# Kernel optimization log

Hardware: AMD Instinct MI355X
Metric: run time of the kernel (lower is better)

## Reference

```python
import jax, jax.numpy as jnp
import numpy as np

EPS_BN = 1e-5
NEG_SLOPE = 0.2
N_GRAPHS = 64


def _gat_layer(x, src, dst, W, att_s, att_d, b, concat):
    # x: [N, Fin]; W: [Fin, H*C]; att_s/att_d: [H, C]; PyG GATConv semantics
    N = x.shape[0]
    H, C = att_s.shape
    h = (x @ W).reshape(N, H, C)                      # [N,H,C]
    a_s = jnp.einsum('nhc,hc->nh', h, att_s)          # per-node src score
    a_d = jnp.einsum('nhc,hc->nh', h, att_d)          # per-node dst score
    e = jax.nn.leaky_relu(a_s[src] + a_d[dst], NEG_SLOPE)  # [E,H]
    m = jax.ops.segment_max(e, dst, num_segments=N)   # segment softmax over incoming edges
    ex = jnp.exp(e - m[dst])
    den = jax.ops.segment_sum(ex, dst, num_segments=N)
    alpha = ex / (den[dst] + 1e-16)                   # [E,H]
    msg = h[src] * alpha[:, :, None]                  # [E,H,C]
    out = jax.ops.segment_sum(msg, dst, num_segments=N)
    out = out.reshape(N, H * C) if concat else out.mean(axis=1)
    return out + b


def _bn(x, g, bt):
    mu = x.mean(axis=0)
    var = x.var(axis=0)
    return (x - mu) * jax.lax.rsqrt(var + EPS_BN) * g + bt


def setup_inputs() -> dict:
    key = jax.random.key(0)
    ks = jax.random.split(key, 32)
    N, E, F = 50000, 800000, 128
    d = {}
    d['x'] = jax.random.normal(ks[0], (N, F), dtype=jnp.float32)
    d['edge_index'] = jax.random.randint(ks[1], (2, E), 0, N, dtype=jnp.int32)
    d['batch'] = jnp.sort(jax.random.randint(ks[2], (N,), 0, N_GRAPHS, dtype=jnp.int32))
    def p(k, shape, fan):
        return jax.random.normal(k, shape, dtype=jnp.float32) * (1.0 / np.sqrt(fan))
    d['W1'] = p(ks[3], (128, 256), 128); d['as1'] = p(ks[4], (4, 64), 64)
    d['ad1'] = p(ks[5], (4, 64), 64); d['b1'] = jnp.zeros((256,), jnp.float32)
    d['W2'] = p(ks[6], (256, 128), 256); d['as2'] = p(ks[7], (4, 32), 32)
    d['ad2'] = p(ks[8], (4, 32), 32); d['b2'] = jnp.zeros((128,), jnp.float32)
    # gat3: 128 -> 64, 1 head, mean
    d['W3'] = p(ks[9], (128, 64), 128); d['as3'] = p(ks[10], (1, 64), 64)
    d['ad3'] = p(ks[11], (1, 64), 64); d['b3'] = jnp.zeros((64,), jnp.float32)
    # batch norms
    d['g1'] = jnp.ones((256,), jnp.float32); d['bt1'] = jnp.zeros((256,), jnp.float32)
    d['g2'] = jnp.ones((128,), jnp.float32); d['bt2'] = jnp.zeros((128,), jnp.float32)
    d['g3'] = jnp.ones((64,), jnp.float32); d['bt3'] = jnp.zeros((64,), jnp.float32)
    # fcn: 64 -> 128 -> 32 -> 2
    d['fw1'] = p(ks[12], (64, 128), 64); d['fb1'] = jnp.zeros((128,), jnp.float32)
    d['fw2'] = p(ks[13], (128, 32), 128); d['fb2'] = jnp.zeros((32,), jnp.float32)
    d['fw3'] = p(ks[14], (32, 2), 32); d['fb3'] = jnp.zeros((2,), jnp.float32)
    return d


def reference(x, edge_index, batch, W1, as1, ad1, b1, W2, as2, ad2, b2,
              W3, as3, ad3, b3, g1, bt1, g2, bt2, g3, bt3,
              fw1, fb1, fw2, fb2, fw3, fb3):
    N = x.shape[0]
    # add self loops (PyG GATConv default)
    loops = jnp.arange(N, dtype=edge_index.dtype)
    src = jnp.concatenate([edge_index[0], loops])
    dst = jnp.concatenate([edge_index[1], loops])
    h = _gat_layer(x, src, dst, W1, as1, ad1, b1, concat=True)
    h = jax.nn.elu(_bn(h, g1, bt1))
    h = _gat_layer(h, src, dst, W2, as2, ad2, b2, concat=True)
    h = jax.nn.elu(_bn(h, g2, bt2))
    h = _gat_layer(h, src, dst, W3, as3, ad3, b3, concat=False)
    h = jax.nn.elu(_bn(h, g3, bt3))
    # global mean pool per graph
    s = jax.ops.segment_sum(h, batch, num_segments=N_GRAPHS)
    cnt = jax.ops.segment_sum(jnp.ones((N,), h.dtype), batch, num_segments=N_GRAPHS)
    pooled = s / jnp.maximum(cnt, 1.0)[:, None]       # [64, 64]
    z = jax.nn.leaky_relu(pooled @ fw1 + fb1, NEG_SLOPE)
    z = jax.nn.leaky_relu(z @ fw2 + fb2, NEG_SLOPE)
    return z @ fw3 + fb3                              # [64, 2]
```

## Files before the change

### kernel.cpp

```cpp
#include <hip/hip_runtime.h>
#include <hip/hip_fp16.h>
#include <math.h>

#define NEG_SLOPE 0.2f
#define BN_NB 128
#define BK_SHIFT 6
#define BK_CAP 2048
#define SC_CHUNK 4096

typedef _Float16 f16x8 __attribute__((ext_vector_type(8)));
typedef float    f32x4 __attribute__((ext_vector_type(4)));


__device__ inline void scan1024_incl(int* tmp) {
    int t = threadIdx.x;
    for (int off = 1; off < 1024; off <<= 1) {
        int vals[4];
#pragma unroll
        for (int k = 0; k < 4; k++) {
            int idx = t + k * 256;
            vals[k] = (idx >= off) ? tmp[idx - off] : 0;
        }
        __syncthreads();
#pragma unroll
        for (int k = 0; k < 4; k++) tmp[t + k * 256] += vals[k];
        __syncthreads();
    }
}

__global__ __launch_bounds__(256) void histA_kernel(const int* __restrict__ dst,
                                                    int* __restrict__ bcnt, int E, int nb) {
    __shared__ int h[1024];
    int t = threadIdx.x;
    for (int i = t; i < 1024; i += 256) h[i] = 0;
    __syncthreads();
    int base = blockIdx.x * SC_CHUNK;
#pragma unroll 4
    for (int k = 0; k < SC_CHUNK / 256; k++) {
        int i = base + t + k * 256;
        if (i < E) atomicAdd(&h[dst[i] >> BK_SHIFT], 1);
    }
    __syncthreads();
    for (int i = t; i < nb; i += 256) if (h[i]) atomicAdd(&bcnt[i], h[i]);
}

__global__ __launch_bounds__(256) void scanAB_kernel(const int* __restrict__ bcnt,
                                                     int* __restrict__ boffs,
                                                     int* __restrict__ gcurs, int nb) {
    __shared__ int tmp[1024];
    int t = threadIdx.x;
    for (int i = t; i < 1024; i += 256) tmp[i] = (i < nb) ? bcnt[i] : 0;
    __syncthreads();
    scan1024_incl(tmp);
    for (int i = t; i < nb; i += 256) {
        int excl = (i == 0) ? 0 : tmp[i - 1];
        boffs[i] = excl;
        gcurs[i] = excl;
    }
    if (t == 0) boffs[nb] = tmp[nb - 1];
}

__global__ __launch_bounds__(256) void scatterB_kernel(const int* __restrict__ src,
                                                       const int* __restrict__ dst,
                                                       int* __restrict__ gcurs,
                                                       unsigned* __restrict__ ebuf,
                                                       int E, int nb) {
    __shared__ int hcnt[1024];
    __shared__ int hcur[1024];
    __shared__ int gbase[1024];
    __shared__ unsigned stage[SC_CHUNK];
    __shared__ unsigned short sbk[SC_CHUNK];
    int t = threadIdx.x;
    int base = blockIdx.x * SC_CHUNK;
    for (int i = t; i < 1024; i += 256) hcnt[i] = 0;
    __syncthreads();
    unsigned pk[SC_CHUNK / 256];
    int bk[SC_CHUNK / 256];
#pragma unroll
    for (int k = 0; k < SC_CHUNK / 256; k++) {
        int i = base + t + k * 256;
        if (i < E) {
            int d = dst[i];
            int s = src[i];
            bk[k] = d >> BK_SHIFT;
            pk[k] = (unsigned)s | ((unsigned)(d & 63) << 16);
            atomicAdd(&hcnt[bk[k]], 1);
        } else bk[k] = -1;
    }
    __syncthreads();
    for (int i = t; i < 1024; i += 256) hcur[i] = hcnt[i];
    __syncthreads();
    scan1024_incl(hcur);
    for (int i = t; i < 1024; i += 256) hcur[i] -= hcnt[i];
    __syncthreads();
#pragma unroll
    for (int k = 0; k < SC_CHUNK / 256; k++) {
        if (bk[k] >= 0) {
            int p = atomicAdd(&hcur[bk[k]], 1);
            stage[p] = pk[k];
            sbk[p] = (unsigned short)bk[k];
        }
    }
    __syncthreads();
    for (int i = t; i < nb; i += 256) {
        int c = hcnt[i];
        gbase[i] = c ? atomicAdd(&gcurs[i], c) : 0;
    }
    __syncthreads();
    int total = E - base; if (total > SC_CHUNK) total = SC_CHUNK;
    for (int i = t; i < total; i += 256) {
        int b = sbk[i];
        int local = i - (hcur[b] - hcnt[b]);
        ebuf[gbase[b] + local] = stage[i];
    }
}

__global__ __launch_bounds__(256) void buildC_kernel(const unsigned* __restrict__ ebuf,
                                                     const int* __restrict__ boffs,
                                                     int* __restrict__ offs,
                                                     int* __restrict__ csrc, int N) {
    __shared__ int ncnt[64], ncur[64];
    __shared__ int npre[65];
    __shared__ unsigned lv[BK_CAP];
    __shared__ int lout[BK_CAP];
    int b = blockIdx.x, t = threadIdx.x;
    int e0 = boffs[b], e1 = boffs[b + 1];
    int cnt = e1 - e0; if (cnt > BK_CAP) cnt = BK_CAP;
    int n0 = b << BK_SHIFT;
    if (t < 64) ncnt[t] = 0;
    __syncthreads();
    for (int i = t; i < cnt; i += 256) {
        unsigned v = ebuf[e0 + i];
        lv[i] = v;
        atomicAdd(&ncnt[v >> 16], 1);
    }
    __syncthreads();
    if (t == 0) {
        int run = 0;
#pragma unroll
        for (int i = 0; i < 64; i++) { npre[i] = run; run += ncnt[i]; }
        npre[64] = run;
    }
    __syncthreads();
    int nEnd = N - n0; if (nEnd > 64) nEnd = 64;
    if (t < nEnd) offs[n0 + t + 1] = e0 + npre[t + 1];
    if (b == 0 && t == 0) offs[0] = 0;
    if (t < 64) ncur[t] = npre[t];
    __syncthreads();
    for (int i = t; i < cnt; i += 256) {
        unsigned v = lv[i];
        int p = atomicAdd(&ncur[v >> 16], 1);
        lout[p] = (int)(v & 0xFFFFu);
    }
    __syncthreads();
    for (int i = t; i < cnt; i += 256) csrc[e0 + i] = lout[i];
}


__device__ inline void swz1(const float* __restrict__ W, __half* __restrict__ Wsw,
                            int Nout, int i) {
    int k = i / Nout, n = i % Nout;
    Wsw[((size_t)(k >> 3) * Nout + n) * 8 + (k & 7)] = __float2half(W[i]);
}

__global__ void prep_kernel(const float* __restrict__ W1, const float* __restrict__ W2,
                            const float* __restrict__ W3,
                            const float* __restrict__ as1, const float* __restrict__ ad1,
                            __half* __restrict__ W1sw, __half* __restrict__ W2sw,
                            __half* __restrict__ W3sw, float* __restrict__ wsd,
                            const float* __restrict__ x, __half* __restrict__ Xh,
                            int castN4) {
    int i = blockIdx.x * 256 + threadIdx.x;
    const int R0 = 128 * 256, R1 = R0 + 256 * 128, R2 = R1 + 128 * 64, R3 = R2 + 1024;
    if (i < R0) { swz1(W1, W1sw, 256, i); }
    else if (i < R1) { swz1(W2, W2sw, 128, i - R0); }
    else if (i < R2) { swz1(W3, W3sw, 64, i - R1); }
    else if (i < R3) {
        int j = (i - R2) >> 7, k = (i - R2) & 127;
        int hh = j & 3;
        const float* att = (j < 4) ? as1 : ad1;
        float s = 0.f;
        for (int c = 0; c < 64; c++) s += W1[k * 256 + hh * 64 + c] * att[hh * 64 + c];
        wsd[i - R2] = s;
    } else {
        int j = i - R3;
        if (j < castN4) {
            float4 v = *(const float4*)(x + (size_t)j * 4);
            __half2 pk[2];
            pk[0] = __floats2half2_rn(v.x, v.y);
            pk[1] = __floats2half2_rn(v.z, v.w);
            *(uint2*)(Xh + (size_t)j * 4) = *(uint2*)pk;
        }
    }
}


__global__ __launch_bounds__(256) void scores1_kernel(const __half* __restrict__ Xh,
                                                      const float* __restrict__ wsd,
                                                      float* __restrict__ a_s,
                                                      float* __restrict__ a_d, int N) {
    int gid = blockIdx.x * 256 + threadIdx.x;
    if (gid >= N * 8) return;
    int n = gid >> 3, j = gid & 7;
    const __half* xp = Xh + (size_t)n * 128;
    const float* wp = wsd + j * 128;
    float s = 0.f;
    for (int k = 0; k < 128; k += 8) {
        uint4 raw = *(const uint4*)(xp + k);
        __half2* hp = (__half2*)&raw;
#pragma unroll
        for (int q = 0; q < 4; q++) {
            float2 f = __half22float2(hp[q]);
            s += f.x * wp[k + 2 * q] + f.y * wp[k + 2 * q + 1];
        }
    }
    if (j < 4) a_s[n * 4 + j] = s; else a_d[n * 4 + (j - 4)] = s;
}


__global__ __launch_bounds__(256) void aggx_kernel(const __half* __restrict__ Xh,
                                                   const float* __restrict__ a_s,
                                                   const float* __restrict__ a_d,
                                                   const int* __restrict__ offs,
                                                   const int* __restrict__ csrc,
                                                   __half* __restrict__ aggx, int N) {
    __shared__ float wbuf[16][16 * 4];
    __shared__ int   sbuf[16][16];
    int tid = threadIdx.x;
    int l16 = tid & 15, grp = tid >> 4;
    int node = blockIdx.x * 16 + grp;
    if (node >= N) return;
    int off = offs[node];
    int deg = offs[node + 1] - off;
    float4 ad4 = *(const float4*)(a_d + (size_t)node * 4);
    float adl[4] = {ad4.x, ad4.y, ad4.z, ad4.w};
    float4 as4 = *(const float4*)(a_s + (size_t)node * 4);
    float asl[4] = {as4.x, as4.y, as4.z, as4.w};
    float wself[4];
#pragma unroll
    for (int h = 0; h < 4; h++) {
        float sc = asl[h] + adl[h];
        sc = sc > 0.f ? sc : NEG_SLOPE * sc;
        wself[h] = __expf(sc);
    }
    float acc[4][8];
    {
        uint4 raw = *(const uint4*)(Xh + (size_t)node * 128 + l16 * 8);
        __half2* p = (__half2*)&raw;
#pragma unroll
        for (int q = 0; q < 4; q++) {
            float2 f = __half22float2(p[q]);
#pragma unroll
            for (int h = 0; h < 4; h++) {
                acc[h][2 * q] = wself[h] * f.x;
                acc[h][2 * q + 1] = wself[h] * f.y;
            }
        }
    }
    float denp[4] = {0.f, 0.f, 0.f, 0.f};
    for (int base = 0; base < deg; base += 16) {
        int i = base + l16;
        if (i < deg) {
            int s = csrc[off + i];
            sbuf[grp][l16] = s;
            float4 t4 = *(const float4*)(a_s + (size_t)s * 4);
            float asv[4] = {t4.x, t4.y, t4.z, t4.w};
#pragma unroll
            for (int h = 0; h < 4; h++) {
                float sc = asv[h] + adl[h];
                sc = sc > 0.f ? sc : NEG_SLOPE * sc;
                float w = __expf(sc);
                wbuf[grp][l16 * 4 + h] = w;
                denp[h] += w;
            }
        }
        asm volatile("s_waitcnt lgkmcnt(0)" ::: "memory");
        int cl = deg - base; if (cl > 16) cl = 16;
#pragma unroll 4
        for (int e = 0; e < cl; e++) {
            int s = sbuf[grp][e];
            float4 wv = *(float4*)&wbuf[grp][e * 4];
            float wa[4] = {wv.x, wv.y, wv.z, wv.w};
            uint4 raw = *(const uint4*)(Xh + (size_t)s * 128 + l16 * 8);
            __half2* p = (__half2*)&raw;
#pragma unroll
            for (int q = 0; q < 4; q++) {
                float2 f = __half22float2(p[q]);
#pragma unroll
                for (int h = 0; h < 4; h++) {
                    acc[h][2 * q] += wa[h] * f.x;
                    acc[h][2 * q + 1] += wa[h] * f.y;
                }
            }
        }
    }
#pragma unroll
    for (int d = 1; d <= 8; d <<= 1)
#pragma unroll
        for (int h = 0; h < 4; h++) denp[h] += __shfl_xor(denp[h], d, 64);
#pragma unroll
    for (int h = 0; h < 4; h++) {
        float inv = 1.0f / (denp[h] + wself[h] + 1e-16f);
        uint4 pk; __half2* q = (__half2*)&pk;
#pragma unroll
        for (int j = 0; j < 4; j++)
            q[j] = __floats2half2_rn(acc[h][2 * j] * inv, acc[h][2 * j + 1] * inv);
        *(uint4*)(aggx + (size_t)node * 512 + h * 128 + l16 * 8) = pk;
    }
}


template <int CH, bool BN, bool SCORES, bool BIAS>
__global__ __launch_bounds__(256) void gemm_mfma(const __half* __restrict__ X,
                                                 const __half* __restrict__ Wsw,
                                                 __half* __restrict__ Yh,
                                                 const float* __restrict__ att_s,
                                                 const float* __restrict__ att_d,
                                                 float* __restrict__ a_s,
                                                 float* __restrict__ a_d,
                                                 const float* __restrict__ partials,
                                                 const float* __restrict__ gbn,
                                                 const float* __restrict__ btbn,
                                                 const float* __restrict__ bias,
                                                 float invN, int aStride, int aOffPerBn,
                                                 int M, int K, int Nout) {
    extern __shared__ char smem_raw[];
    __half* Bs = (__half*)smem_raw;
    float* ssc = (float*)(smem_raw + (size_t)K * 64 * 2);
    float* ssb = ssc + K;
    int tid = threadIdx.x;
    int wave = tid >> 6, lane = tid & 63;
    int bm = blockIdx.x * 128;
    int bn = blockIdx.y * 64;

    if (BN && tid < K) {
        float ssum = 0.f, qsum = 0.f;
        for (int b = 0; b < BN_NB; b++) {
            ssum += partials[(size_t)b * 2 * K + tid];
            qsum += partials[(size_t)b * 2 * K + K + tid];
        }
        float mu = ssum * invN;
        float var = qsum * invN - mu * mu;
        float sc = gbn[tid] * rsqrtf(var + 1e-5f);
        ssc[tid] = sc;
        ssb[tid] = btbn[tid] - mu * sc;
    }

    int ktCount = K >> 3;
    int totalVec = ktCount * 64;
    for (int i = tid; i < totalVec; i += 256) {
        int kt = i >> 6, off = i & 63;
        ((uint4*)Bs)[i] = *(const uint4*)(Wsw + ((size_t)kt * Nout + bn + off) * 8);
    }
    __syncthreads();

    int quad = lane >> 4, l15 = lane & 15;
    int row0 = bm + wave * 32 + l15;
    bool r0ok = (row0 < M), r1ok = (row0 + 16 < M);
    int aOff = blockIdx.y * aOffPerBn;
    const __half* a0p = X + (size_t)row0 * aStride + aOff + quad * 8;
    const __half* a1p = a0p + (size_t)16 * aStride;

    f32x4 acc[2][4] = {};
    for (int kstep = 0; kstep < K; kstep += 32) {
        f16x8 a0 = {}, a1 = {};
        if (r0ok) a0 = *(const f16x8*)(a0p + kstep);
        if (r1ok) a1 = *(const f16x8*)(a1p + kstep);
        if (BN) {
            int c0 = kstep + quad * 8;
#pragma unroll
            for (int j = 0; j < 8; j++) {
                float sc = ssc[c0 + j], sb = ssb[c0 + j];
                float v0 = (float)a0[j] * sc + sb;
                v0 = v0 > 0.f ? v0 : (__expf(v0) - 1.0f);
                a0[j] = (_Float16)v0;
                float v1 = (float)a1[j] * sc + sb;
                v1 = v1 > 0.f ? v1 : (__expf(v1) - 1.0f);
                a1[j] = (_Float16)v1;
            }
        }
        int ktbase = (kstep >> 3) + quad;
#pragma unroll
        for (int nt = 0; nt < 4; nt++) {
            f16x8 b = *(const f16x8*)(Bs + ((size_t)ktbase * 64 + nt * 16 + l15) * 8);
            acc[0][nt] = __builtin_amdgcn_mfma_f32_16x16x32_f16(a0, b, acc[0][nt], 0, 0, 0);
            acc[1][nt] = __builtin_amdgcn_mfma_f32_16x16x32_f16(a1, b, acc[1][nt], 0, 0, 0);
        }
    }

    float bv[4];
    if (BIAS) {
#pragma unroll
        for (int nt = 0; nt < 4; nt++) bv[nt] = bias[bn + nt * 16 + l15];
    }

#pragma unroll
    for (int mt = 0; mt < 2; mt++) {
#pragma unroll
        for (int r = 0; r < 4; r++) {
            int row = bm + wave * 32 + mt * 16 + quad * 4 + r;
            if (row < M) {
#pragma unroll
                for (int nt = 0; nt < 4; nt++) {
                    float v = acc[mt][nt][r];
                    if (BIAS) v += bv[nt];
                    Yh[(size_t)row * Nout + bn + nt * 16 + l15] = __float2half(v);
                }
            }
        }
    }

    if (SCORES) {
        constexpr int LH = 64 / CH;
        const int H = Nout / CH;
        float as_l[4], ad_l[4];
#pragma unroll
        for (int nt = 0; nt < 4; nt++) {
            int gcol = bn + nt * 16 + l15;
            as_l[nt] = att_s[gcol];
            ad_l[nt] = att_d[gcol];
        }
        float ps[2][4][LH], pd[2][4][LH];
#pragma unroll
        for (int mt = 0; mt < 2; mt++)
#pragma unroll
            for (int r = 0; r < 4; r++)
#pragma unroll
                for (int lh = 0; lh < LH; lh++) { ps[mt][r][lh] = 0.f; pd[mt][r][lh] = 0.f; }
#pragma unroll
        for (int mt = 0; mt < 2; mt++)
#pragma unroll
            for (int nt = 0; nt < 4; nt++) {
                int lh = (nt * 16) / CH;
#pragma unroll
                for (int r = 0; r < 4; r++) {
                    ps[mt][r][lh] += acc[mt][nt][r] * as_l[nt];
                    pd[mt][r][lh] += acc[mt][nt][r] * ad_l[nt];
                }
            }
#pragma unroll
        for (int d = 1; d <= 8; d <<= 1) {
#pragma unroll
            for (int mt = 0; mt < 2; mt++)
#pragma unroll
                for (int r = 0; r < 4; r++)
#pragma unroll
                    for (int lh = 0; lh < LH; lh++) {
                        ps[mt][r][lh] += __shfl_xor(ps[mt][r][lh], d, 64);
                        pd[mt][r][lh] += __shfl_xor(pd[mt][r][lh], d, 64);
                    }
        }
        if (l15 == 0) {
#pragma unroll
            for (int mt = 0; mt < 2; mt++)
#pragma unroll
                for (int r = 0; r < 4; r++) {
                    int row = bm + wave * 32 + mt * 16 + quad * 4 + r;
                    if (row < M) {
#pragma unroll
                        for (int lh = 0; lh < LH; lh++) {
                            int ghead = bn / CH + lh;
                            a_s[(size_t)row * H + ghead] = ps[mt][r][lh];
                            a_d[(size_t)row * H + ghead] = pd[mt][r][lh];
                        }
                    }
                }
        }
    }
}


template <int H, int C>
__global__ __launch_bounds__(256) void agg_kernel(const __half* __restrict__ h,
                                                  const float* __restrict__ a_s,
                                                  const float* __restrict__ a_d,
                                                  const int* __restrict__ offs,
                                                  const int* __restrict__ csrc,
                                                  const float* __restrict__ bias,
                                                  __half* __restrict__ out, int N) {
    const int HC = H * C;
    const int CPL = HC / 16;
    __shared__ float wbuf[16][16 * H];
    __shared__ int   sbuf[16][16];
    int tid = threadIdx.x;
    int l16 = tid & 15;
    int grp = tid >> 4;
    int node = blockIdx.x * 16 + grp;
    if (node >= N) return;
    int off = offs[node];
    int deg = offs[node + 1] - off;
    int mych = l16 * CPL;
    int mh   = mych / C;

    float adl[H];
#pragma unroll
    for (int hh = 0; hh < H; hh++) adl[hh] = a_d[node * H + hh];

    float acc[CPL];
    float sc_self = a_s[node * H + mh] + adl[mh];
    sc_self = sc_self > 0.f ? sc_self : NEG_SLOPE * sc_self;
    float w_self = __expf(sc_self);
    {
        const __half* hp = h + (size_t)node * HC + mych;
        if (CPL == 8) {
            uint4 r0 = *(const uint4*)hp;
            __half2* p0 = (__half2*)&r0;
#pragma unroll
            for (int j = 0; j < 4; j++) {
                float2 f = __half22float2(p0[j]);
                acc[2 * j] = w_self * f.x; acc[2 * j + 1] = w_self * f.y;
            }
        } else {
            uint2 r0 = *(const uint2*)hp;
            __half2* p0 = (__half2*)&r0;
#pragma unroll
            for (int j = 0; j < 2; j++) {
                float2 f = __half22float2(p0[j]);
                acc[2 * j] = w_self * f.x; acc[2 * j + 1] = w_self * f.y;
            }
        }
    }

    float denp[H];
#pragma unroll
    for (int hh = 0; hh < H; hh++) denp[hh] = 0.f;

    for (int base = 0; base < deg; base += 16) {
        int i = base + l16;
        if (i < deg) {
            int s = csrc[off + i];
            sbuf[grp][l16] = s;
            float asv[H];
            if (H == 4) {
                float4 t4 = *(const float4*)(a_s + (size_t)s * 4);
                asv[0] = t4.x; asv[1] = t4.y; asv[2] = t4.z; asv[3] = t4.w;
            } else {
                asv[0] = a_s[s];
            }
#pragma unroll
            for (int hh = 0; hh < H; hh++) {
                float sc = asv[hh] + adl[hh];
                sc = sc > 0.f ? sc : NEG_SLOPE * sc;
                float w = __expf(sc);
                wbuf[grp][l16 * H + hh] = w;
                denp[hh] += w;
            }
        }
        asm volatile("s_waitcnt lgkmcnt(0)" ::: "memory");
        int cl = deg - base; if (cl > 16) cl = 16;
#pragma unroll 4
        for (int e = 0; e < cl; e++) {
            int s = sbuf[grp][e];
            float w = wbuf[grp][e * H + mh];
            const __half* hp = h + (size_t)s * HC + mych;
            if (CPL == 8) {
                uint4 r0 = *(const uint4*)hp;
                __half2* p0 = (__half2*)&r0;
#pragma unroll
                for (int j = 0; j < 4; j++) {
                    float2 f = __half22float2(p0[j]);
                    acc[2 * j] += w * f.x; acc[2 * j + 1] += w * f.y;
                }
            } else {
                uint2 r0 = *(const uint2*)hp;
                __half2* p0 = (__half2*)&r0;
#pragma unroll
                for (int j = 0; j < 2; j++) {
                    float2 f = __half22float2(p0[j]);
                    acc[2 * j] += w * f.x; acc[2 * j + 1] += w * f.y;
                }
            }
        }
    }
#pragma unroll
    for (int d = 1; d <= 8; d <<= 1) {
#pragma unroll
        for (int hh = 0; hh < H; hh++)
            denp[hh] += __shfl_xor(denp[hh], d, 64);
    }
    float inv = 1.0f / (denp[mh] + w_self + 1e-16f);
    {
        __half* op = out + (size_t)node * HC + mych;
        if (CPL == 8) {
            uint4 pk;
            __half2* q = (__half2*)&pk;
#pragma unroll
            for (int j = 0; j < 4; j++)
                q[j] = __floats2half2_rn(acc[2 * j] * inv + bias[mych + 2 * j],
                                         acc[2 * j + 1] * inv + bias[mych + 2 * j + 1]);
            *(uint4*)op = pk;
        } else {
            uint2 pk;
            __half2* q = (__half2*)&pk;
#pragma unroll
            for (int j = 0; j < 2; j++)
                q[j] = __floats2half2_rn(acc[2 * j] * inv + bias[mych + 2 * j],
                                         acc[2 * j + 1] * inv + bias[mych + 2 * j + 1]);
            *(uint2*)op = pk;
        }
    }
}


__global__ __launch_bounds__(256) void bnstats_kernel(const __half* __restrict__ buf,
                                                      float* __restrict__ partials,
                                                      int N, int Cc) {
    __shared__ float lds_s[2048], lds_q[2048];
    int t = threadIdx.x;
    int tpr = Cc >> 3;
    int rpb = 256 / tpr;
    int r   = t / tpr;
    int c8  = (t % tpr) * 8;
    int row = blockIdx.x * rpb + r;
    int stride = gridDim.x * rpb;
    float s[8] = {}, q[8] = {};
    for (int n = row; n < N; n += stride) {
        uint4 raw = *(const uint4*)(buf + (size_t)n * Cc + c8);
        __half2* hp = (__half2*)&raw;
#pragma unroll
        for (int j = 0; j < 4; j++) {
            float2 f = __half22float2(hp[j]);
            s[2 * j] += f.x; q[2 * j] += f.x * f.x;
            s[2 * j + 1] += f.y; q[2 * j + 1] += f.y * f.y;
        }
    }
#pragma unroll
    for (int j = 0; j < 8; j++) {
        lds_s[r * Cc + c8 + j] = s[j];
        lds_q[r * Cc + c8 + j] = q[j];
    }
    __syncthreads();
    for (int off = rpb >> 1; off >= 1; off >>= 1) {
        if (r < off) {
#pragma unroll
            for (int j = 0; j < 8; j++) {
                lds_s[r * Cc + c8 + j] += lds_s[(r + off) * Cc + c8 + j];
                lds_q[r * Cc + c8 + j] += lds_q[(r + off) * Cc + c8 + j];
            }
        }
        __syncthreads();
    }
    if (r == 0) {
        float* p = partials + (size_t)blockIdx.x * 2 * Cc;
#pragma unroll
        for (int j = 0; j < 8; j++) {
            p[c8 + j] = lds_s[c8 + j];
            p[Cc + c8 + j] = lds_q[c8 + j];
        }
    }
}


__global__ __launch_bounds__(512) void poolmlp_kernel(const __half* __restrict__ h,
                                                      const int* __restrict__ batch,
                                                      const float* __restrict__ partials,
                                                      const float* __restrict__ gbn,
                                                      const float* __restrict__ btbn,
                                                      float invN,
                                                      const float* __restrict__ fw1, const float* __restrict__ fb1,
                                                      const float* __restrict__ fw2, const float* __restrict__ fb2,
                                                      const float* __restrict__ fw3, const float* __restrict__ fb3,
                                                      float* __restrict__ out, int N) {
    int g = blockIdx.x;
    int t = threadIdx.x;
    __shared__ float ssc[64], ssb[64];
    if (t < 64) {
        float ssum = 0.f, qsum = 0.f;
        for (int b = 0; b < BN_NB; b++) {
            ssum += partials[(size_t)b * 128 + t];
            qsum += partials[(size_t)b * 128 + 64 + t];
        }
        float mu = ssum * invN;
        float var = qsum * invN - mu * mu;
        float sc = gbn[t] * rsqrtf(var + 1e-5f);
        ssc[t] = sc;
        ssb[t] = btbn[t] - mu * sc;
    }
    int lo = 0, hi = N;
    while (lo < hi) { int mid = (lo + hi) >> 1; if (batch[mid] < g) lo = mid + 1; else hi = mid; }
    int s = lo;
    hi = N;
    while (lo < hi) { int mid = (lo + hi) >> 1; if (batch[mid] < g + 1) lo = mid + 1; else hi = mid; }
    int e = lo;
    __syncthreads();

    int rg = t >> 3;
    int c8 = (t & 7) * 8;
    float sc[8], sb[8];
#pragma unroll
    for (int j = 0; j < 8; j++) { sc[j] = ssc[c8 + j]; sb[j] = ssb[c8 + j]; }
    float acc[8] = {};
    for (int n = s + rg; n < e; n += 64) {
        uint4 raw = *(const uint4*)(h + (size_t)n * 64 + c8);
        __half2* hp = (__half2*)&raw;
#pragma unroll
        for (int j = 0; j < 4; j++) {
            float2 f = __half22float2(hp[j]);
            float va = f.x * sc[2 * j] + sb[2 * j];
            acc[2 * j] += va > 0.f ? va : (__expf(va) - 1.0f);
            float vb = f.y * sc[2 * j + 1] + sb[2 * j + 1];
            acc[2 * j + 1] += vb > 0.f ? vb : (__expf(vb) - 1.0f);
        }
    }
    __shared__ float red[64 * 64];
#pragma unroll
    for (int j = 0; j < 8; j++) red[rg * 64 + c8 + j] = acc[j];
    __syncthreads();
    for (int off = 32; off >= 1; off >>= 1) {
        if (rg < off) {
#pragma unroll
            for (int j = 0; j < 8; j++)
                red[rg * 64 + c8 + j] += red[(rg + off) * 64 + c8 + j];
        }
        __syncthreads();
    }
    __shared__ float pm[64];
    __shared__ float z1[128];
    __shared__ float z2[32];
    if (t < 64) pm[t] = red[t] / fmaxf((float)(e - s), 1.0f);
    __syncthreads();
    if (t < 128) {
        float v = fb1[t];
        for (int k = 0; k < 64; k++) v += pm[k] * fw1[k * 128 + t];
        z1[t] = v > 0.f ? v : NEG_SLOPE * v;
    }
    __syncthreads();
    if (t < 32) {
        float v = fb2[t];
        for (int k = 0; k < 128; k++) v += z1[k] * fw2[k * 32 + t];
        z2[t] = v > 0.f ? v : NEG_SLOPE * v;
    }
    __syncthreads();
    if (t < 2) {
        float v = fb3[t];
        for (int k = 0; k < 32; k++) v += z2[k] * fw3[k * 2 + t];
        out[g * 2 + t] = v;
    }
}


extern "C" void kernel_launch(void* const* d_in, const int* in_sizes, int n_in,
                              void* d_out, int out_size, void* d_ws, size_t ws_size,
                              hipStream_t stream) {
    const float* x   = (const float*)d_in[0];
    const int*   ei  = (const int*)d_in[1];
    const int*   batch = (const int*)d_in[2];
    const float* W1  = (const float*)d_in[3];
    const float* as1 = (const float*)d_in[4];
    const float* ad1 = (const float*)d_in[5];
    const float* b1  = (const float*)d_in[6];
    const float* W2  = (const float*)d_in[7];
    const float* as2 = (const float*)d_in[8];
    const float* ad2 = (const float*)d_in[9];
    const float* b2  = (const float*)d_in[10];
    const float* W3  = (const float*)d_in[11];
    const float* as3 = (const float*)d_in[12];
    const float* ad3 = (const float*)d_in[13];
    const float* b3  = (const float*)d_in[14];
    const float* g1  = (const float*)d_in[15];
    const float* bt1 = (const float*)d_in[16];
    const float* g2  = (const float*)d_in[17];
    const float* bt2 = (const float*)d_in[18];
    const float* g3  = (const float*)d_in[19];
    const float* bt3 = (const float*)d_in[20];
    const float* fw1 = (const float*)d_in[21];
    const float* fb1 = (const float*)d_in[22];
    const float* fw2 = (const float*)d_in[23];
    const float* fb2 = (const float*)d_in[24];
    const float* fw3 = (const float*)d_in[25];
    const float* fb3 = (const float*)d_in[26];

    const int N = in_sizes[0] / 128;
    const int E = in_sizes[1] / 2;
    const int* srcv = ei;
    const int* dstv = ei + E;
    const int nb = (N + 63) >> 6;

    float* fws   = (float*)d_ws;
    float* ar1F  = fws;
    float* ar2F  = ar1F + (size_t)N * 128;
    float* a_s   = ar2F + (size_t)N * 256;
    float* a_d   = a_s + (size_t)N * 4;
    float* part1 = a_d + (size_t)N * 4;
    float* part2 = part1 + BN_NB * 512;
    float* part3 = part2 + BN_NB * 256;
    int*   bcnt  = (int*)(part3 + BN_NB * 128);
    int*   boffs = bcnt + 1024;
    int*   gcurs = boffs + 1025;
    int*   offs  = gcurs + 1024;
    int*   csrc  = offs + N + 1;
    unsigned* ebuf = (unsigned*)(csrc + E);
    float* wswF  = (float*)(ebuf + E);
    __half* W1sw = (__half*)wswF;
    __half* W2sw = W1sw + 128 * 256;
    __half* W3sw = W2sw + 256 * 128;
    float* wsd   = (float*)(W3sw + 128 * 64);

    __half* Xh   = (__half*)ar1F;
    __half* out1 = (__half*)ar1F;
    __half* h3   = (__half*)ar1F;
    __half* out3 = (__half*)ar1F + (size_t)N * 64;
    __half* aggx = (__half*)ar2F;
    __half* h2   = (__half*)ar2F;
    __half* out2 = (__half*)ar2F + (size_t)N * 256;

    dim3 blk(256);
    const int scGrid = (E + SC_CHUNK - 1) / SC_CHUNK;

    hipMemsetAsync(bcnt, 0, 1024 * 4, stream);

    histA_kernel<<<scGrid, blk, 0, stream>>>(dstv, bcnt, E, nb);
    scanAB_kernel<<<1, blk, 0, stream>>>(bcnt, boffs, gcurs, nb);
    scatterB_kernel<<<scGrid, blk, 0, stream>>>(srcv, dstv, gcurs, ebuf, E, nb);
    buildC_kernel<<<nb, blk, 0, stream>>>(ebuf, boffs, offs, csrc, N);

    {
        int castN4 = N * 32;
        int total = 128 * 256 + 256 * 128 + 128 * 64 + 1024 + castN4;
        prep_kernel<<<(total + 255) / 256, blk, 0, stream>>>(W1, W2, W3, as1, ad1,
                                                             W1sw, W2sw, W3sw, wsd,
                                                             x, Xh, castN4);
    }

    {
        scores1_kernel<<<((size_t)N * 8 + 255) / 256, blk, 0, stream>>>(Xh, wsd, a_s, a_d, N);
        aggx_kernel<<<(N + 15) / 16, blk, 0, stream>>>(Xh, a_s, a_d, offs, csrc, aggx, N);
        dim3 grid((N + 127) / 128, 4);
        gemm_mfma<64, false, false, true><<<grid, blk, 128 * 128, stream>>>(
            aggx, W1sw, out1, nullptr, nullptr, nullptr, nullptr,
            nullptr, nullptr, nullptr, b1, 0.f, 512, 128, N, 128, 256);
        bnstats_kernel<<<BN_NB, blk, 0, stream>>>(out1, part1, N, 256);
    }
    {
        dim3 grid((N + 127) / 128, 2);
        gemm_mfma<32, true, true, false><<<grid, blk, 256 * 128 + 2 * 256 * 4, stream>>>(
            out1, W2sw, h2, as2, ad2, a_s, a_d, part1, g1, bt1, nullptr,
            1.0f / N, 256, 0, N, 256, 128);
        agg_kernel<4, 32><<<(N + 15) / 16, blk, 0, stream>>>(h2, a_s, a_d, offs, csrc, b2, out2, N);
        bnstats_kernel<<<BN_NB, blk, 0, stream>>>(out2, part2, N, 128);
    }
    {
        dim3 grid((N + 127) / 128, 1);
        gemm_mfma<64, true, true, false><<<grid, blk, 128 * 128 + 2 * 128 * 4, stream>>>(
            out2, W3sw, h3, as3, ad3, a_s, a_d, part2, g2, bt2, nullptr,
            1.0f / N, 128, 0, N, 128, 64);
        agg_kernel<1, 64><<<(N + 15) / 16, blk, 0, stream>>>(h3, a_s, a_d, offs, csrc, b3, out3, N);
        bnstats_kernel<<<BN_NB, blk, 0, stream>>>(out3, part3, N, 64);
    }

    poolmlp_kernel<<<64, 512, 0, stream>>>(out3, batch, part3, g3, bt3, 1.0f / N,
                                           fw1, fb1, fw2, fb2, fw3, fb3,
                                           (float*)d_out, N);
}
```

Baseline: 414.4 us.

## Fuse layer-1 aggregation with per-head MFMA projection in one kernel

Merges the layer-1 attention aggregation kernel with the following projection GEMM. Each block aggregates 16 nodes into a shared-memory tile (4 heads x 128 features in fp16), then multiplies that tile by W1 with 16x16x32 MFMA instructions and writes out1 with the bias added. This drops the N x 512 fp16 aggx round trip through global memory and one launch. In exchange, every block re-reads the W1 slices from global or L2, the small 16-row tile underuses the MFMA units, and the extra shared memory may lower occupancy. Buffer aliasing is remapped to match.

```diff
diff --git a/kernel.cpp b/kernel.cpp
--- a/kernel.cpp
+++ b/kernel.cpp
@@ -218,94 +218,130 @@
 }
 
 
-__global__ __launch_bounds__(256) void aggx_kernel(const __half* __restrict__ Xh,
-                                                   const float* __restrict__ a_s,
-                                                   const float* __restrict__ a_d,
-                                                   const int* __restrict__ offs,
-                                                   const int* __restrict__ csrc,
-                                                   __half* __restrict__ aggx, int N) {
+__global__ __launch_bounds__(256) void aggx_gemm1_kernel(const __half* __restrict__ Xh,
+                                                         const float* __restrict__ a_s,
+                                                         const float* __restrict__ a_d,
+                                                         const int* __restrict__ offs,
+                                                         const int* __restrict__ csrc,
+                                                         const __half* __restrict__ W1sw,
+                                                         const float* __restrict__ b1,
+                                                         __half* __restrict__ out1, int N) {
     __shared__ float wbuf[16][16 * 4];
     __shared__ int   sbuf[16][16];
+    __shared__ __half Ast[16][520];
     int tid = threadIdx.x;
     int l16 = tid & 15, grp = tid >> 4;
-    int node = blockIdx.x * 16 + grp;
-    if (node >= N) return;
-    int off = offs[node];
-    int deg = offs[node + 1] - off;
-    float4 ad4 = *(const float4*)(a_d + (size_t)node * 4);
-    float adl[4] = {ad4.x, ad4.y, ad4.z, ad4.w};
-    float4 as4 = *(const float4*)(a_s + (size_t)node * 4);
-    float asl[4] = {as4.x, as4.y, as4.z, as4.w};
-    float wself[4];
-#pragma unroll
-    for (int h = 0; h < 4; h++) {
-        float sc = asl[h] + adl[h];
-        sc = sc > 0.f ? sc : NEG_SLOPE * sc;
-        wself[h] = __expf(sc);
-    }
-    float acc[4][8];
-    {
-        uint4 raw = *(const uint4*)(Xh + (size_t)node * 128 + l16 * 8);
-        __half2* p = (__half2*)&raw;
-#pragma unroll
-        for (int q = 0; q < 4; q++) {
-            float2 f = __half22float2(p[q]);
-#pragma unroll
-            for (int h = 0; h < 4; h++) {
-                acc[h][2 * q] = wself[h] * f.x;
-                acc[h][2 * q + 1] = wself[h] * f.y;
-            }
-        }
-    }
-    float denp[4] = {0.f, 0.f, 0.f, 0.f};
-    for (int base = 0; base < deg; base += 16) {
-        int i = base + l16;
-        if (i < deg) {
-            int s = csrc[off + i];
-            sbuf[grp][l16] = s;
-            float4 t4 = *(const float4*)(a_s + (size_t)s * 4);
-            float asv[4] = {t4.x, t4.y, t4.z, t4.w};
-#pragma unroll
-            for (int h = 0; h < 4; h++) {
-                float sc = asv[h] + adl[h];
-                sc = sc > 0.f ? sc : NEG_SLOPE * sc;
-                float w = __expf(sc);
-                wbuf[grp][l16 * 4 + h] = w;
-                denp[h] += w;
-            }
-        }
-        asm volatile("s_waitcnt lgkmcnt(0)" ::: "memory");
-        int cl = deg - base; if (cl > 16) cl = 16;
-#pragma unroll 4
-        for (int e = 0; e < cl; e++) {
-            int s = sbuf[grp][e];
-            float4 wv = *(float4*)&wbuf[grp][e * 4];
-            float wa[4] = {wv.x, wv.y, wv.z, wv.w};
-            uint4 raw = *(const uint4*)(Xh + (size_t)s * 128 + l16 * 8);
+    int nodeBase = blockIdx.x * 16;
+    int node = nodeBase + grp;
+    bool act = node < N;
+
+    if (act) {
+        int off = offs[node];
+        int deg = offs[node + 1] - off;
+        float4 ad4 = *(const float4*)(a_d + (size_t)node * 4);
+        float adl[4] = {ad4.x, ad4.y, ad4.z, ad4.w};
+        float4 as4 = *(const float4*)(a_s + (size_t)node * 4);
+        float asl[4] = {as4.x, as4.y, as4.z, as4.w};
+        float wself[4];
+#pragma unroll
+        for (int h = 0; h < 4; h++) {
+            float sc = asl[h] + adl[h];
+            sc = sc > 0.f ? sc : NEG_SLOPE * sc;
+            wself[h] = __expf(sc);
+        }
+        float acc[4][8];
+        {
+            uint4 raw = *(const uint4*)(Xh + (size_t)node * 128 + l16 * 8);
             __half2* p = (__half2*)&raw;
 #pragma unroll
             for (int q = 0; q < 4; q++) {
                 float2 f = __half22float2(p[q]);
 #pragma unroll
                 for (int h = 0; h < 4; h++) {
-                    acc[h][2 * q] += wa[h] * f.x;
-                    acc[h][2 * q + 1] += wa[h] * f.y;
+                    acc[h][2 * q] = wself[h] * f.x;
+                    acc[h][2 * q + 1] = wself[h] * f.y;
                 }
             }
         }
-    }
-#pragma unroll
-    for (int d = 1; d <= 8; d <<= 1)
-#pragma unroll
-        for (int h = 0; h < 4; h++) denp[h] += __shfl_xor(denp[h], d, 64);
-#pragma unroll
-    for (int h = 0; h < 4; h++) {
-        float inv = 1.0f / (denp[h] + wself[h] + 1e-16f);
-        uint4 pk; __half2* q = (__half2*)&pk;
-#pragma unroll
-        for (int j = 0; j < 4; j++)
-            q[j] = __floats2half2_rn(acc[h][2 * j] * inv, acc[h][2 * j + 1] * inv);
-        *(uint4*)(aggx + (size_t)node * 512 + h * 128 + l16 * 8) = pk;
+        float denp[4] = {0.f, 0.f, 0.f, 0.f};
+        for (int base = 0; base < deg; base += 16) {
+            int i = base + l16;
+            if (i < deg) {
+                int s = csrc[off + i];
+                sbuf[grp][l16] = s;
+                float4 t4 = *(const float4*)(a_s + (size_t)s * 4);
+                float asv[4] = {t4.x, t4.y, t4.z, t4.w};
+#pragma unroll
+                for (int h = 0; h < 4; h++) {
+                    float sc = asv[h] + adl[h];
+                    sc = sc > 0.f ? sc : NEG_SLOPE * sc;
+                    float w = __expf(sc);
+                    wbuf[grp][l16 * 4 + h] = w;
+                    denp[h] += w;
+                }
+            }
+            asm volatile("s_waitcnt lgkmcnt(0)" ::: "memory");
+            int cl = deg - base; if (cl > 16) cl = 16;
+#pragma unroll 4
+            for (int e = 0; e < cl; e++) {
+                int s = sbuf[grp][e];
+                float4 wv = *(float4*)&wbuf[grp][e * 4];
+                float wa[4] = {wv.x, wv.y, wv.z, wv.w};
+                uint4 raw = *(const uint4*)(Xh + (size_t)s * 128 + l16 * 8);
+                __half2* p = (__half2*)&raw;
+#pragma unroll
+                for (int q = 0; q < 4; q++) {
+                    float2 f = __half22float2(p[q]);
+#pragma unroll
+                    for (int h = 0; h < 4; h++) {
+                        acc[h][2 * q] += wa[h] * f.x;
+                        acc[h][2 * q + 1] += wa[h] * f.y;
+                    }
+                }
+            }
+        }
+#pragma unroll
+        for (int d = 1; d <= 8; d <<= 1)
+#pragma unroll
+            for (int h = 0; h < 4; h++) denp[h] += __shfl_xor(denp[h], d, 64);
+#pragma unroll
+        for (int h = 0; h < 4; h++) {
+            float inv = 1.0f / (denp[h] + wself[h] + 1e-16f);
+            uint4 pk; __half2* q = (__half2*)&pk;
+#pragma unroll
+            for (int j = 0; j < 4; j++)
+                q[j] = __floats2half2_rn(acc[h][2 * j] * inv, acc[h][2 * j + 1] * inv);
+            *(uint4*)&Ast[grp][h * 128 + l16 * 8] = pk;
+        }
+    }
+    __syncthreads();
+
+    int wave = tid >> 6, lane = tid & 63;
+    int quad = lane >> 4, l15 = lane & 15;
+    f32x4 accg[4] = {};
+#pragma unroll
+    for (int kstep = 0; kstep < 4; kstep++) {
+        f16x8 a = *(const f16x8*)&Ast[l15][wave * 128 + kstep * 32 + quad * 8];
+        int kt = kstep * 4 + quad;
+#pragma unroll
+        for (int nt = 0; nt < 4; nt++) {
+            int col = wave * 64 + nt * 16 + l15;
+            f16x8 b = *(const f16x8*)(W1sw + ((size_t)kt * 256 + col) * 8);
+            accg[nt] = __builtin_amdgcn_mfma_f32_16x16x32_f16(a, b, accg[nt], 0, 0, 0);
+        }
+    }
+    float bv[4];
+#pragma unroll
+    for (int nt = 0; nt < 4; nt++) bv[nt] = b1[wave * 64 + nt * 16 + l15];
+#pragma unroll
+    for (int r = 0; r < 4; r++) {
+        int n2 = nodeBase + quad * 4 + r;
+        if (n2 < N) {
+#pragma unroll
+            for (int nt = 0; nt < 4; nt++)
+                out1[(size_t)n2 * 256 + wave * 64 + nt * 16 + l15] =
+                    __float2half(accg[nt][r] + bv[nt]);
+        }
     }
 }
 
@@ -797,12 +833,11 @@
     float* wsd   = (float*)(W3sw + 128 * 64);
 
     __half* Xh   = (__half*)ar1F;
-    __half* out1 = (__half*)ar1F;
+    __half* out1 = (__half*)ar2F;
+    __half* h2   = (__half*)ar1F;
+    __half* out2 = (__half*)ar2F;
     __half* h3   = (__half*)ar1F;
-    __half* out3 = (__half*)ar1F + (size_t)N * 64;
-    __half* aggx = (__half*)ar2F;
-    __half* h2   = (__half*)ar2F;
-    __half* out2 = (__half*)ar2F + (size_t)N * 256;
+    __half* out3 = (__half*)ar2F;
 
     dim3 blk(256);
     const int scGrid = (E + SC_CHUNK - 1) / SC_CHUNK;
@@ -824,11 +859,8 @@
 
     {
         scores1_kernel<<<((size_t)N * 8 + 255) / 256, blk, 0, stream>>>(Xh, wsd, a_s, a_d, N);
-        aggx_kernel<<<(N + 15) / 16, blk, 0, stream>>>(Xh, a_s, a_d, offs, csrc, aggx, N);
-        dim3 grid((N + 127) / 128, 4);
-        gemm_mfma<64, false, false, true><<<grid, blk, 128 * 128, stream>>>(
-            aggx, W1sw, out1, nullptr, nullptr, nullptr, nullptr,
-            nullptr, nullptr, nullptr, b1, 0.f, 512, 128, N, 128, 256);
+        aggx_gemm1_kernel<<<(N + 15) / 16, blk, 0, stream>>>(Xh, a_s, a_d, offs, csrc,
+                                                             W1sw, b1, out1, N);
         bnstats_kernel<<<BN_NB, blk, 0, stream>>>(out1, part1, N, 256);
     }
     {
```

Measured after the change: 403.7 us. 2.6% less time.
